# Kernel tuning notes

Measured on AMD Instinct MI355X. Metric: run time of the kernel, lower is better.

## Reference

```python
import jax, jax.numpy as jnp
import numpy as np

EPS = 1e-5


def conv2d(x, w, b, stride=1, pad=1):
    out = jax.lax.conv_general_dilated(
        x, w, (stride, stride), [(pad, pad), (pad, pad)],
        dimension_numbers=('NCHW', 'OIHW', 'NCHW'))
    return out + b[None, :, None, None]


def bn_inf(x, gamma, beta, mean, var):
    inv = gamma / jnp.sqrt(var + EPS)
    return x * inv[None, :, None, None] + (beta - mean * inv)[None, :, None, None]


def deform_conv(x, offset, weight, stride, pad, dil):
    # x: [B,Ci,H,W], offset: [B,2*K*K,Ho,Wo] (dy,dx interleaved per kernel pos),
    # weight: [Co,Ci,K,K]. torchvision DeformConv2d v1 semantics, no bias.
    B, Ci, H, W = x.shape
    Co, _, K, _ = weight.shape
    KK = K * K
    Ho = (H + 2 * pad - dil * (K - 1) - 1) // stride + 1
    Wo = (W + 2 * pad - dil * (K - 1) - 1) // stride + 1
    dy = offset[:, 0::2]  # [B,KK,Ho,Wo]
    dx = offset[:, 1::2]
    ky, kx = jnp.meshgrid(jnp.arange(K), jnp.arange(K), indexing='ij')
    ky = ky.reshape(KK).astype(x.dtype)
    kx = kx.reshape(KK).astype(x.dtype)
    base_y = (jnp.arange(Ho) * stride - pad).astype(x.dtype)
    base_x = (jnp.arange(Wo) * stride - pad).astype(x.dtype)
    ys = base_y[None, None, :, None] + (ky * dil)[None, :, None, None] + dy
    xs = base_x[None, None, None, :] + (kx * dil)[None, :, None, None] + dx
    y0 = jnp.floor(ys)
    x0 = jnp.floor(xs)
    fy = ys - y0
    fx = xs - x0

    def gather(img, iy, ix):
        # img: [Ci,H,W]; iy, ix: [KK,Ho,Wo] float integer-valued coords
        valid = (iy >= 0) & (iy < H) & (ix >= 0) & (ix < W)
        iyc = jnp.clip(iy, 0, H - 1).astype(jnp.int32)
        ixc = jnp.clip(ix, 0, W - 1).astype(jnp.int32)
        v = img[:, iyc, ixc]  # [Ci,KK,Ho,Wo]
        return v * valid[None].astype(img.dtype)

    def sample_one(img, y0b, x0b, fyb, fxb):
        w00 = (1 - fyb) * (1 - fxb)
        w01 = (1 - fyb) * fxb
        w10 = fyb * (1 - fxb)
        w11 = fyb * fxb
        s = (gather(img, y0b, x0b) * w00[None]
             + gather(img, y0b, x0b + 1) * w01[None]
             + gather(img, y0b + 1, x0b) * w10[None]
             + gather(img, y0b + 1, x0b + 1) * w11[None])
        return s  # [Ci,KK,Ho,Wo]

    sampled = jax.vmap(sample_one)(x, y0, x0, fy, fx)  # [B,Ci,KK,Ho,Wo]
    return jnp.einsum('oik,bikhw->bohw', weight.reshape(Co, Ci, KK), sampled)


def setup_inputs() -> dict:
    key = jax.random.key(0)
    ks = jax.random.split(key, 16)
    B, C, H, W = 8, 128, 64, 64
    d = dict(
        x=jax.random.normal(ks[0], (B, C, H, W), jnp.float32),
        w_off1=jax.random.normal(ks[1], (18, C, 3, 3), jnp.float32) * 0.01,
        b_off1=jnp.zeros((18,), jnp.float32),
        w_dc1=jax.random.normal(ks[2], (C, C, 3, 3), jnp.float32) * 0.05,
        g1=jnp.ones((C,), jnp.float32),
        beta1=jnp.zeros((C,), jnp.float32),
        m1=jax.random.normal(ks[3], (C,), jnp.float32) * 0.1,
        v1=jax.random.uniform(ks[4], (C,), jnp.float32) + 0.5,
        w_off2=jax.random.normal(ks[5], (18, C, 3, 3), jnp.float32) * 0.01,
        b_off2=jnp.zeros((18,), jnp.float32),
        w_dc2=jax.random.normal(ks[6], (C, C, 3, 3), jnp.float32) * 0.05,
        g2=jnp.ones((C,), jnp.float32),
        beta2=jnp.zeros((C,), jnp.float32),
        m2=jax.random.normal(ks[7], (C,), jnp.float32) * 0.1,
        v2=jax.random.uniform(ks[8], (C,), jnp.float32) + 0.5,
    )
    return d


def reference(x, w_off1, b_off1, w_dc1, g1, beta1, m1, v1,
              w_off2, b_off2, w_dc2, g2, beta2, m2, v2):
    # BasicBlock6 forward (stride=1, in_planes==planes => identity shortcut)
    off1 = conv2d(x, w_off1, b_off1, stride=1, pad=1)
    out = jax.nn.relu(bn_inf(deform_conv(x, off1, w_dc1, 1, 2, 2), g1, beta1, m1, v1))
    off2 = conv2d(out, w_off2, b_off2, stride=1, pad=1)
    out = bn_inf(deform_conv(out, off2, w_dc2, 1, 2, 2), g2, beta2, m2, v2)
    out = out + x  # identity shortcut
    return jax.nn.relu(out)
```

## Files before the change

kernel.cpp:

```cpp
#include <hip/hip_runtime.h>
#include <hip/hip_bf16.h>

#define CH   128
#define HH   64
#define WW   64
#define OFFC 18

typedef __attribute__((ext_vector_type(8))) short bf16x8;
typedef __attribute__((ext_vector_type(4))) short bf16x4;
typedef __attribute__((ext_vector_type(4))) float f32x4;

static __device__ __forceinline__ unsigned short f2bf(float f) {
    __hip_bfloat16 h = __float2bfloat16(f);
    return *reinterpret_cast<unsigned short*>(&h);
}
static __device__ __forceinline__ float bf2f(unsigned short u) {
    union { unsigned int i; float f; } x; x.i = ((unsigned int)u) << 16;
    return x.f;
}

__global__ __launch_bounds__(256) void prep_kernel(
    const float* __restrict__ x, unsigned short* __restrict__ xh,
    const float* __restrict__ wdc1, const float* __restrict__ wdc2,
    const float* __restrict__ wof1, const float* __restrict__ wof2,
    unsigned short* __restrict__ wpk1, unsigned short* __restrict__ wpk2,
    unsigned short* __restrict__ wpo1, unsigned short* __restrict__ wpo2)
{
    __shared__ float s[CH][WW + 1];
    int blk = blockIdx.x;
    int tid = threadIdx.x;

    if (blk < 1152) {
        const float* w = (blk < 576) ? wdc1 : wdc2;
        unsigned short* wp = (blk < 576) ? wpk1 : wpk2;
        int id = (blk % 576) * 256 + tid;
        int j    = id & 7;
        int lane = (id >> 3) & 63;
        int ot   = (id >> 9) & 7;
        int kk   = (id >> 12) & 3;
        int k    = id >> 14;
        int o = ot * 16 + (lane & 15);
        int i = kk * 32 + (lane >> 4) * 8 + j;
        wp[id] = f2bf(w[(o * CH + i) * 9 + k]);
        return;
    }
    if (blk < 1440) {
        const float* w = (blk < 1296) ? wof1 : wof2;
        unsigned short* wp = (blk < 1296) ? wpo1 : wpo2;
        int id = ((blk - 1152) % 144) * 256 + tid;
        int j    = id & 7;
        int lane = (id >> 3) & 63;
        int mt   = (id >> 9) & 1;
        int kk   = (id >> 10) & 3;
        int k    = id >> 12;
        int o = mt * 16 + (lane & 15);
        int i = kk * 32 + (lane >> 4) * 8 + j;
        wp[id] = (o < OFFC) ? f2bf(w[(o * CH + i) * 9 + k]) : (unsigned short)0;
        return;
    }

    int nb = blk - 1440;
    const float* xb = x + ((size_t)(nb >> 6) * CH * HH + (nb & 63)) * WW;

    int c_off = tid >> 4, w0 = (tid & 15) * 4;
    #pragma unroll
    for (int it = 0; it < 8; ++it) {
        int c = it * 16 + c_off;
        float4 vv = *(const float4*)&xb[(size_t)c * HH * WW + w0];
        s[c][w0] = vv.x; s[c][w0 + 1] = vv.y; s[c][w0 + 2] = vv.z; s[c][w0 + 3] = vv.w;
    }
    __syncthreads();

    int w = tid & 63, c0 = (tid >> 6) * 32;
    unsigned short* dst = xh + ((size_t)nb * WW + w) * CH + c0;
    unsigned short tmp[32];
    #pragma unroll
    for (int j = 0; j < 32; ++j) tmp[j] = f2bf(s[c0 + j][w]);
    #pragma unroll
    for (int q = 0; q < 4; ++q)
        *(bf16x8*)(dst + q * 8) = *(const bf16x8*)(tmp + q * 8);
}

__global__ __launch_bounds__(256) void off_conv_mfma_kernel(
    const unsigned short* __restrict__ xh,
    const unsigned short* __restrict__ wpo,
    const float* __restrict__ bias,
    unsigned short* __restrict__ offh)
{
    int wgid = blockIdx.x;
    int blk  = (wgid & 7) * 64 + (wgid >> 3);
    int b = blk >> 6, oh = blk & 63;
    int tid = threadIdx.x;
    int lane = tid & 63;
    int nt = tid >> 6;
    int nl = lane & 15;
    int kg = lane >> 4;

    f32x4 acc0 = {0.f, 0.f, 0.f, 0.f}, acc1 = {0.f, 0.f, 0.f, 0.f};
    const unsigned short* xb = xh + (size_t)b * HH * WW * CH;

    for (int k = 0; k < 9; ++k) {
        int ky = k / 3, kx = k - ky * 3;
        int ih = oh - 1 + ky;
        if (ih < 0 || ih >= HH) continue;
        int iw = nt * 16 + nl + kx - 1;
        bool valid = (iw >= 0) && (iw < WW);
        const unsigned short* row = xb + ((size_t)ih * WW + (valid ? iw : 0)) * CH + kg * 8;
        const unsigned short* wk = wpo + (size_t)k * 4096;
        #pragma unroll
        for (int kk = 0; kk < 4; ++kk) {
            bf16x8 bfrag = {0, 0, 0, 0, 0, 0, 0, 0};
            if (valid) bfrag = *(const bf16x8*)(row + kk * 32);
            bf16x8 a0 = *(const bf16x8*)(wk + (kk * 2 + 0) * 512 + lane * 8);
            bf16x8 a1 = *(const bf16x8*)(wk + (kk * 2 + 1) * 512 + lane * 8);
            acc0 = __builtin_amdgcn_mfma_f32_16x16x32_bf16(a0, bfrag, acc0, 0, 0, 0);
            acc1 = __builtin_amdgcn_mfma_f32_16x16x32_bf16(a1, bfrag, acc1, 0, 0, 0);
        }
    }

    int ow = nt * 16 + nl;
    #pragma unroll
    for (int r = 0; r < 4; ++r) {
        int co = kg * 4 + r;
        offh[(((size_t)b * OFFC + co) * HH + oh) * WW + ow] = f2bf(acc0[r] + bias[co]);
    }
    if (kg == 0) {
        #pragma unroll
        for (int r = 0; r < 2; ++r) {
            int co = 16 + r;
            offh[(((size_t)b * OFFC + co) * HH + oh) * WW + ow] = f2bf(acc1[r] + bias[co]);
        }
    }
}

__global__ __launch_bounds__(256, 4) void deform_mfma2_kernel(
    const unsigned short* __restrict__ xh,
    const unsigned short* __restrict__ offh,
    const unsigned short* __restrict__ wpk,
    const float* __restrict__ g, const float* __restrict__ beta,
    const float* __restrict__ m, const float* __restrict__ v,
    const float* __restrict__ residual,
    unsigned short* __restrict__ out_h,
    float* __restrict__ out_f)
{
    __shared__ unsigned short sB[32 * 128];
    __shared__ float off_s[2 * 9][32];

    int wgid = blockIdx.x;
    int blk  = (wgid & 7) * 128 + (wgid >> 3);
    int owh = blk & 1, oh = (blk >> 1) & 63, b = blk >> 7;
    int ow0 = owh * 32;
    int tid = threadIdx.x, lane = tid & 63, wv = tid >> 6;

    int s_ow = tid >> 3;
    int ci0  = (tid & 7) * 16;
    int ow_g = ow0 + s_ow;

    const unsigned short* xb = xh + (size_t)b * HH * WW * CH;

    for (int i = tid; i < 2 * 9 * 32; i += 256) {
        int co = i >> 5, owl = i & 31;
        off_s[co][owl] =
            bf2f(offh[(((size_t)b * OFFC + co) * HH + oh) * WW + ow0 + owl]);
    }
    __syncthreads();

    f32x4 acc[2][2];
    #pragma unroll
    for (int a = 0; a < 2; ++a)
        #pragma unroll
        for (int q = 0; q < 2; ++q) acc[a][q] = (f32x4){0.f, 0.f, 0.f, 0.f};

    for (int k = 0; k < 9; ++k) {
        int ky = k / 3, kx = k - ky * 3;

        float dy = off_s[2 * k][s_ow];
        float dx = off_s[2 * k + 1][s_ow];
        float ys = (float)(oh - 2 + ky * 2) + dy;
        float xs = (float)(ow_g - 2 + kx * 2) + dx;
        float y0f = floorf(ys), x0f = floorf(xs);
        float fy = ys - y0f, fx = xs - x0f;
        int y0 = (int)y0f, x0i = (int)x0f;
        int y1 = y0 + 1, x1 = x0i + 1;
        bool vy0 = (y0 >= 0) & (y0 < HH), vy1 = (y1 >= 0) & (y1 < HH);
        bool vx0 = (x0i >= 0) & (x0i < WW), vx1 = (x1 >= 0) & (x1 < WW);
        int y0c = min(max(y0, 0), HH - 1), y1c = min(max(y1, 0), HH - 1);
        int x0c = min(max(x0i, 0), WW - 1), x1c = min(max(x1, 0), WW - 1);
        float cw0 = (1.f - fy) * (1.f - fx) * ((vy0 && vx0) ? 1.f : 0.f);
        float cw1 = (1.f - fy) * fx         * ((vy0 && vx1) ? 1.f : 0.f);
        float cw2 = fy * (1.f - fx)         * ((vy1 && vx0) ? 1.f : 0.f);
        float cw3 = fy * fx                 * ((vy1 && vx1) ? 1.f : 0.f);

        const unsigned short* p0 = xb + ((size_t)(y0c * WW + x0c)) * CH + ci0;
        const unsigned short* p1 = xb + ((size_t)(y0c * WW + x1c)) * CH + ci0;
        const unsigned short* p2 = xb + ((size_t)(y1c * WW + x0c)) * CH + ci0;
        const unsigned short* p3 = xb + ((size_t)(y1c * WW + x1c)) * CH + ci0;

        int base = s_ow * 256 + ci0 * 2;
        int swz  = (s_ow & 7) << 4;
        #pragma unroll
        for (int q = 0; q < 2; ++q) {
            bf16x8 g0 = *(const bf16x8*)(p0 + q * 8);
            bf16x8 g1 = *(const bf16x8*)(p1 + q * 8);
            bf16x8 g2 = *(const bf16x8*)(p2 + q * 8);
            bf16x8 g3 = *(const bf16x8*)(p3 + q * 8);
            union { bf16x8 v8; unsigned short u[8]; } wu;
            #pragma unroll
            for (int j = 0; j < 8; ++j) {
                float val = cw0 * bf2f((unsigned short)g0[j])
                          + cw1 * bf2f((unsigned short)g1[j])
                          + cw2 * bf2f((unsigned short)g2[j])
                          + cw3 * bf2f((unsigned short)g3[j]);
                wu.u[j] = f2bf(val);
            }
            *(bf16x8*)((char*)sB + ((base + q * 16) ^ swz)) = wu.v8;
        }
        __syncthreads();

        const unsigned short* wk = wpk + (size_t)k * 16384;
        #pragma unroll
        for (int kk = 0; kk < 4; ++kk) {
            bf16x8 a0 = *(const bf16x8*)(wk + (kk * 8 + 2 * wv)     * 512 + lane * 8);
            bf16x8 a1 = *(const bf16x8*)(wk + (kk * 8 + 2 * wv + 1) * 512 + lane * 8);
            #pragma unroll
            for (int owt = 0; owt < 2; ++owt) {
                int owl = owt * 16 + (lane & 15);
                int rbyte = (owl * 256 + (kk * 32 + (lane >> 4) * 8) * 2)
                            ^ ((owl & 7) << 4);
                bf16x8 bfv = *(const bf16x8*)((const char*)sB + rbyte);
                acc[0][owt] = __builtin_amdgcn_mfma_f32_16x16x32_bf16(
                                  a0, bfv, acc[0][owt], 0, 0, 0);
                acc[1][owt] = __builtin_amdgcn_mfma_f32_16x16x32_bf16(
                                  a1, bfv, acc[1][owt], 0, 0, 0);
            }
        }
        __syncthreads();
    }

    if (out_h != nullptr) {
        #pragma unroll
        for (int otl = 0; otl < 2; ++otl) {
            int ob = (2 * wv + otl) * 16 + (lane >> 4) * 4;
            float inv[4], sh[4];
            #pragma unroll
            for (int r = 0; r < 4; ++r) {
                int o = ob + r;
                float iv = g[o] / sqrtf(v[o] + 1e-5f);
                inv[r] = iv; sh[r] = beta[o] - m[o] * iv;
            }
            #pragma unroll
            for (int owt = 0; owt < 2; ++owt) {
                int ow = ow0 + owt * 16 + (lane & 15);
                union { bf16x4 v4; unsigned short u[4]; } pk;
                #pragma unroll
                for (int r = 0; r < 4; ++r) {
                    float val = acc[otl][owt][r] * inv[r] + sh[r];
                    pk.u[r] = f2bf(fmaxf(val, 0.f));
                }
                *(bf16x4*)(out_h + ((size_t)(b * HH + oh) * WW + ow) * CH + ob) = pk.v4;
            }
        }
    } else {
        #pragma unroll
        for (int otl = 0; otl < 2; ++otl) {
            #pragma unroll
            for (int r = 0; r < 4; ++r) {
                int o = (2 * wv + otl) * 16 + (lane >> 4) * 4 + r;
                float iv = g[o] / sqrtf(v[o] + 1e-5f);
                float sh = beta[o] - m[o] * iv;
                #pragma unroll
                for (int owt = 0; owt < 2; ++owt) {
                    int ow = ow0 + owt * 16 + (lane & 15);
                    size_t idx = (((size_t)b * CH + o) * HH + oh) * WW + ow;
                    float val = acc[otl][owt][r] * iv + sh + residual[idx];
                    out_f[idx] = fmaxf(val, 0.f);
                }
            }
        }
    }
}

extern "C" void kernel_launch(void* const* d_in, const int* in_sizes, int n_in,
                              void* d_out, int out_size, void* d_ws, size_t ws_size,
                              hipStream_t stream)
{
    const float* x      = (const float*)d_in[0];
    const float* w_off1 = (const float*)d_in[1];
    const float* b_off1 = (const float*)d_in[2];
    const float* w_dc1  = (const float*)d_in[3];
    const float* g1     = (const float*)d_in[4];
    const float* beta1  = (const float*)d_in[5];
    const float* m1     = (const float*)d_in[6];
    const float* v1     = (const float*)d_in[7];
    const float* w_off2 = (const float*)d_in[8];
    const float* b_off2 = (const float*)d_in[9];
    const float* w_dc2  = (const float*)d_in[10];
    const float* g2     = (const float*)d_in[11];
    const float* beta2  = (const float*)d_in[12];
    const float* m2     = (const float*)d_in[13];
    const float* v2     = (const float*)d_in[14];
    float* out = (float*)d_out;

    char* ws = (char*)d_ws;
    unsigned short* xh    = (unsigned short*)ws;
    unsigned short* out1h = (unsigned short*)(ws + 8388608);
    unsigned short* offh  = (unsigned short*)(ws + 16777216);
    unsigned short* wpk1  = (unsigned short*)(ws + 17956864);
    unsigned short* wpk2  = (unsigned short*)(ws + 18251776);
    unsigned short* wpo1  = (unsigned short*)(ws + 18546688);
    unsigned short* wpo2  = (unsigned short*)(ws + 18620416);

    prep_kernel<<<1952, 256, 0, stream>>>(x, xh, w_dc1, w_dc2, w_off1, w_off2,
                                          wpk1, wpk2, wpo1, wpo2);

    off_conv_mfma_kernel<<<512, 256, 0, stream>>>(xh, wpo1, b_off1, offh);
    deform_mfma2_kernel<<<1024, 256, 0, stream>>>(xh, offh, wpk1,
                                                  g1, beta1, m1, v1,
                                                  nullptr, out1h, nullptr);
    off_conv_mfma_kernel<<<512, 256, 0, stream>>>(out1h, wpo2, b_off2, offh);
    deform_mfma2_kernel<<<1024, 256, 0, stream>>>(out1h, offh, wpk2,
                                                  g2, beta2, m2, v2,
                                                  x, nullptr, out);
}
```

Before: 96.69 us.

## Process a full output row per 512-thread block in deformable conv

```diff
diff --git a/kernel.cpp b/kernel.cpp
--- a/kernel.cpp
+++ b/kernel.cpp
@@ -133,7 +133,7 @@
     }
 }
 
-__global__ __launch_bounds__(256, 4) void deform_mfma2_kernel(
+__global__ __launch_bounds__(512, 4) void deform_row_kernel(
     const unsigned short* __restrict__ xh,
     const unsigned short* __restrict__ offh,
     const unsigned short* __restrict__ wpk,
@@ -143,33 +143,29 @@
     unsigned short* __restrict__ out_h,
     float* __restrict__ out_f)
 {
-    __shared__ unsigned short sB[32 * 128];
-    __shared__ float off_s[2 * 9][32];
+    __shared__ unsigned short sB[64 * 128];
+    __shared__ float off_s[OFFC][WW];
 
     int wgid = blockIdx.x;
-    int blk  = (wgid & 7) * 128 + (wgid >> 3);
-    int owh = blk & 1, oh = (blk >> 1) & 63, b = blk >> 7;
-    int ow0 = owh * 32;
+    int blk  = (wgid & 7) * 64 + (wgid >> 3);
+    int b = blk >> 6, oh = blk & 63;
     int tid = threadIdx.x, lane = tid & 63, wv = tid >> 6;
 
     int s_ow = tid >> 3;
     int ci0  = (tid & 7) * 16;
-    int ow_g = ow0 + s_ow;
 
     const unsigned short* xb = xh + (size_t)b * HH * WW * CH;
 
-    for (int i = tid; i < 2 * 9 * 32; i += 256) {
-        int co = i >> 5, owl = i & 31;
+    for (int i = tid; i < OFFC * WW; i += 512) {
+        int co = i >> 6, owl = i & 63;
         off_s[co][owl] =
-            bf2f(offh[(((size_t)b * OFFC + co) * HH + oh) * WW + ow0 + owl]);
+            bf2f(offh[(((size_t)b * OFFC + co) * HH + oh) * WW + owl]);
     }
     __syncthreads();
 
-    f32x4 acc[2][2];
-    #pragma unroll
-    for (int a = 0; a < 2; ++a)
-        #pragma unroll
-        for (int q = 0; q < 2; ++q) acc[a][q] = (f32x4){0.f, 0.f, 0.f, 0.f};
+    f32x4 acc[4];
+    #pragma unroll
+    for (int q = 0; q < 4; ++q) acc[q] = (f32x4){0.f, 0.f, 0.f, 0.f};
 
     for (int k = 0; k < 9; ++k) {
         int ky = k / 3, kx = k - ky * 3;
@@ -177,7 +173,7 @@
         float dy = off_s[2 * k][s_ow];
         float dx = off_s[2 * k + 1][s_ow];
         float ys = (float)(oh - 2 + ky * 2) + dy;
-        float xs = (float)(ow_g - 2 + kx * 2) + dx;
+        float xs = (float)(s_ow - 2 + kx * 2) + dx;
         float y0f = floorf(ys), x0f = floorf(xs);
         float fy = ys - y0f, fx = xs - x0f;
         int y0 = (int)y0f, x0i = (int)x0f;
@@ -220,61 +216,51 @@
         const unsigned short* wk = wpk + (size_t)k * 16384;
         #pragma unroll
         for (int kk = 0; kk < 4; ++kk) {
-            bf16x8 a0 = *(const bf16x8*)(wk + (kk * 8 + 2 * wv)     * 512 + lane * 8);
-            bf16x8 a1 = *(const bf16x8*)(wk + (kk * 8 + 2 * wv + 1) * 512 + lane * 8);
+            bf16x8 a = *(const bf16x8*)(wk + (size_t)(kk * 8 + wv) * 512 + lane * 8);
             #pragma unroll
-            for (int owt = 0; owt < 2; ++owt) {
+            for (int owt = 0; owt < 4; ++owt) {
                 int owl = owt * 16 + (lane & 15);
                 int rbyte = (owl * 256 + (kk * 32 + (lane >> 4) * 8) * 2)
                             ^ ((owl & 7) << 4);
                 bf16x8 bfv = *(const bf16x8*)((const char*)sB + rbyte);
-                acc[0][owt] = __builtin_amdgcn_mfma_f32_16x16x32_bf16(
-                                  a0, bfv, acc[0][owt], 0, 0, 0);
-                acc[1][owt] = __builtin_amdgcn_mfma_f32_16x16x32_bf16(
-                                  a1, bfv, acc[1][owt], 0, 0, 0);
+                acc[owt] = __builtin_amdgcn_mfma_f32_16x16x32_bf16(
+                               a, bfv, acc[owt], 0, 0, 0);
             }
         }
         __syncthreads();
     }
 
+    int ob = wv * 16 + (lane >> 4) * 4;
+    float inv[4], sh[4];
+    #pragma unroll
+    for (int r = 0; r < 4; ++r) {
+        int o = ob + r;
+        float iv = g[o] / sqrtf(v[o] + 1e-5f);
+        inv[r] = iv; sh[r] = beta[o] - m[o] * iv;
+    }
+
     if (out_h != nullptr) {
         #pragma unroll
-        for (int otl = 0; otl < 2; ++otl) {
-            int ob = (2 * wv + otl) * 16 + (lane >> 4) * 4;
-            float inv[4], sh[4];
+        for (int owt = 0; owt < 4; ++owt) {
+            int ow = owt * 16 + (lane & 15);
+            union { bf16x4 v4; unsigned short u[4]; } pk;
             #pragma unroll
             for (int r = 0; r < 4; ++r) {
-                int o = ob + r;
-                float iv = g[o] / sqrtf(v[o] + 1e-5f);
-                inv[r] = iv; sh[r] = beta[o] - m[o] * iv;
+                float val = acc[owt][r] * inv[r] + sh[r];
+                pk.u[r] = f2bf(fmaxf(val, 0.f));
             }
+            *(bf16x4*)(out_h + ((size_t)(b * HH + oh) * WW + ow) * CH + ob) = pk.v4;
+        }
+    } else {
+        #pragma unroll
+        for (int r = 0; r < 4; ++r) {
+            int o = ob + r;
             #pragma unroll
-            for (int owt = 0; owt < 2; ++owt) {
-                int ow = ow0 + owt * 16 + (lane & 15);
-                union { bf16x4 v4; unsigned short u[4]; } pk;
-                #pragma unroll
-                for (int r = 0; r < 4; ++r) {
-                    float val = acc[otl][owt][r] * inv[r] + sh[r];
-                    pk.u[r] = f2bf(fmaxf(val, 0.f));
-                }
-                *(bf16x4*)(out_h + ((size_t)(b * HH + oh) * WW + ow) * CH + ob) = pk.v4;
-            }
-        }
-    } else {
-        #pragma unroll
-        for (int otl = 0; otl < 2; ++otl) {
-            #pragma unroll
-            for (int r = 0; r < 4; ++r) {
-                int o = (2 * wv + otl) * 16 + (lane >> 4) * 4 + r;
-                float iv = g[o] / sqrtf(v[o] + 1e-5f);
-                float sh = beta[o] - m[o] * iv;
-                #pragma unroll
-                for (int owt = 0; owt < 2; ++owt) {
-                    int ow = ow0 + owt * 16 + (lane & 15);
-                    size_t idx = (((size_t)b * CH + o) * HH + oh) * WW + ow;
-                    float val = acc[otl][owt][r] * iv + sh + residual[idx];
-                    out_f[idx] = fmaxf(val, 0.f);
-                }
+            for (int owt = 0; owt < 4; ++owt) {
+                int ow = owt * 16 + (lane & 15);
+                size_t idx = (((size_t)b * CH + o) * HH + oh) * WW + ow;
+                float val = acc[owt][r] * inv[r] + sh[r] + residual[idx];
+                out_f[idx] = fmaxf(val, 0.f);
             }
         }
     }
@@ -314,11 +300,11 @@
                                           wpk1, wpk2, wpo1, wpo2);
 
     off_conv_mfma_kernel<<<512, 256, 0, stream>>>(xh, wpo1, b_off1, offh);
-    deform_mfma2_kernel<<<1024, 256, 0, stream>>>(xh, offh, wpk1,
-                                                  g1, beta1, m1, v1,
-                                                  nullptr, out1h, nullptr);
+    deform_row_kernel<<<512, 512, 0, stream>>>(xh, offh, wpk1,
+                                               g1, beta1, m1, v1,
+                                               nullptr, out1h, nullptr);
     off_conv_mfma_kernel<<<512, 256, 0, stream>>>(out1h, wpo2, b_off2, offh);
-    deform_mfma2_kernel<<<1024, 256, 0, stream>>>(out1h, offh, wpk2,
-                                                  g2, beta2, m2, v2,
-                                                  x, nullptr, out);
-}
+    deform_row_kernel<<<512, 512, 0, stream>>>(out1h, offh, wpk2,
+                                               g2, beta2, m2, v2,
+                                               x, nullptr, out);
+}
```

New measurement: 95.20 us. Within noise of the previous version (-1.5%).
